# Performance work log

Hardware: AMD Instinct MI355X
Metric: run time of the kernel (lower is better)

Reference implementation:

```python
import jax, jax.numpy as jnp
import numpy as np
from jax import lax

# Conv3d(in_dim, in_dim, kernel=(1,3,3), padding=(0,1,1)) == per-time-slice 3x3 conv mixing channels

def _conv3d(x, w, b):
    # x: [B, C, T, W, H], w: [O, I, 1, 3, 3], b: [O]
    y = lax.conv_general_dilated(
        x, w,
        window_strides=(1, 1, 1),
        padding=[(0, 0), (1, 1), (1, 1)],
        dimension_numbers=("NCDHW", "OIDHW", "NCDHW"),
    )
    return y + b[None, :, None, None, None]


def setup_inputs() -> dict:
    key = jax.random.key(0)
    ks = jax.random.split(key, 8)
    B, C, T, W, H = 8, 64, 16, 64, 64
    fan = C * 1 * 3 * 3
    bound = 1.0 / np.sqrt(fan)  # torch Conv3d default init range
    x = jax.random.normal(ks[0], (B, C, T, W, H), dtype=jnp.float32)
    wq = jax.random.uniform(ks[1], (C, C, 1, 3, 3), jnp.float32, -bound, bound)
    wk = jax.random.uniform(ks[2], (C, C, 1, 3, 3), jnp.float32, -bound, bound)
    wv = jax.random.uniform(ks[3], (C, C, 1, 3, 3), jnp.float32, -bound, bound)
    bq = jax.random.uniform(ks[4], (C,), jnp.float32, -bound, bound)
    bk = jax.random.uniform(ks[5], (C,), jnp.float32, -bound, bound)
    bv = jax.random.uniform(ks[6], (C,), jnp.float32, -bound, bound)
    # torch init is gamma=0 (identity output); use nonzero so reference exercises the full path
    gamma = jax.random.normal(ks[7], (1,), dtype=jnp.float32) * 0.1
    return {"x": x, "wq": wq, "wk": wk, "wv": wv,
            "bq": bq, "bk": bk, "bv": bv, "gamma": gamma}


def reference(x, wq, wk, wv, bq, bk, bv, gamma):
    B, C, T, W, H = x.shape
    WH = W * H
    q = _conv3d(x, wq, bq).reshape(B, C, T, WH)
    k = _conv3d(x, wk, bk).reshape(B, C, T, WH)
    v = _conv3d(x, wv, bv).reshape(B, C, T, WH)
    # Original: (q[...,:,None] @ k[...,None,:]) @ v[...,:,None]  -> rank-1 energy, no softmax.
    # Exact reassociation: out_i = q_i * sum_j(k_j * v_j), avoiding the [WH, WH] matrix.
    s = jnp.sum(k * v, axis=-1, keepdims=True)  # [B, C, T, 1]
    out = (q * s).reshape(B, C, T, W, H)
    return gamma[0] * out + x
```

## Files before the change

### kernel.cpp

```cpp
#include <hip/hip_runtime.h>
#include <hip/hip_bf16.h>
#include <stdint.h>

typedef __attribute__((ext_vector_type(8))) short bf16x8;
typedef __attribute__((ext_vector_type(4))) float f32x4v;
typedef __attribute__((ext_vector_type(16))) float f32x16;

#define CH_STRIDE 65536

__device__ __forceinline__ uint16_t f2bf(float f) {
  uint32_t u = __builtin_bit_cast(uint32_t, f);
  u = (u + 0x7FFFu + ((u >> 16) & 1u)) >> 16;
  return (uint16_t)u;
}
__device__ __forceinline__ float bf2f(uint32_t b) {
  return __builtin_bit_cast(float, b << 16);
}
__device__ __forceinline__ uint16_t cvt_bf(float f) {
  return __builtin_bit_cast(uint16_t, __float2bfloat16(f));
}

#define MFMA32(a, b, c) __builtin_amdgcn_mfma_f32_32x32x16_bf16(a, b, c, 0, 0, 0)
#define WAIT0 asm volatile("s_waitcnt vmcnt(0) lgkmcnt(0)" ::: "memory")
#define BAR __builtin_amdgcn_s_barrier()
#define SCHED0 __builtin_amdgcn_sched_barrier(0)

#define LDSX6  (6 * 8 * 66 * 16)
#define LDSX10 (10 * 8 * 66 * 16)

__device__ __forceinline__ void gld16(const void* g, void* l) {
  __builtin_amdgcn_global_load_lds(
      (const __attribute__((address_space(1))) uint32_t*)g,
      (__attribute__((address_space(3))) uint32_t*)l, 16, 0, 0);
}

__device__ __forceinline__ bf16x8 ldx(const uint8_t* ldsx, int row, int oct, int ci) {
  return *(const bf16x8*)(ldsx + (uint32_t)((row * 8 + oct) * 66 + ci) * 16u);
}
__device__ __forceinline__ bf16x8 ldw_kv(const uint8_t* ldsw, int oct, int rowloc) {
  return *(const bf16x8*)(ldsw + (uint32_t)(oct * 128 + rowloc) * 16u);
}
__device__ __forceinline__ bf16x8 ldw_q(const uint8_t* ldsw, int oct, int row) {
  return *(const bf16x8*)(ldsw + (uint32_t)(oct * 64 + row) * 16u);
}

__device__ __forceinline__ void stage_unit(uint8_t* ldsx, const float* xs, int w0, int u) {
  int row = u >> 7, oct = (u >> 4) & 7, g = u & 15;
  int w = w0 - 1 + row;
  uint32_t base = (uint32_t)((row * 8 + oct) * 66 + 4 * g + 1) * 16u;
  if ((unsigned)w < 64u) {
    const float* p = xs + (size_t)(oct * 8) * CH_STRIDE + w * 64 + 4 * g;
    f32x4v v[8];
    #pragma unroll
    for (int j = 0; j < 8; ++j) v[j] = *(const f32x4v*)(p + (size_t)j * CH_STRIDE);
    #pragma unroll
    for (int c = 0; c < 4; ++c) {
      bf16x8 frag;
      #pragma unroll
      for (int q = 0; q < 4; ++q) {
        frag[2 * q]     = (short)cvt_bf(v[2 * q][c]);
        frag[2 * q + 1] = (short)cvt_bf(v[2 * q + 1][c]);
      }
      *(bf16x8*)(ldsx + base + (uint32_t)c * 16u) = frag;
    }
  } else {
    bf16x8 z = {};
    #pragma unroll
    for (int c = 0; c < 4; ++c) *(bf16x8*)(ldsx + base + (uint32_t)c * 16u) = z;
  }
}
__device__ __forceinline__ void stage_halo(uint8_t* ldsx, int tid, int nrow) {
  if (tid < nrow * 16) {
    int row = tid >> 4, rem = tid & 15;
    int oct = rem >> 1, side = rem & 1;
    bf16x8 z = {};
    *(bf16x8*)(ldsx + (uint32_t)((row * 8 + oct) * 66 + side * 65) * 16u) = z;
  }
}

__global__ void prep_weights(const float* __restrict__ wq, const float* __restrict__ wk,
                             const float* __restrict__ wv, uint16_t* __restrict__ wout) {
  int i = blockIdx.x * 256 + threadIdx.x;
  if (i >= 110592) return;
  if (i < 36864) {
    int tap = i >> 12, oct = (i >> 9) & 7, row = (i >> 3) & 63, j = i & 7;
    wout[i] = f2bf(wq[(row * 64 + oct * 8 + j) * 9 + tap]);
  } else {
    int m = i - 36864;
    int tap = m >> 13, oct = (m >> 10) & 7, rl = (m >> 3) & 127, j = m & 7;
    const float* src = (rl < 64) ? wk : wv;
    wout[i] = f2bf(src[((rl & 63) * 64 + oct * 8 + j) * 9 + tap]);
  }
}

__global__ __launch_bounds__(512, 2) void kv_s_kernel(
    const float* __restrict__ x, const uint16_t* __restrict__ wkv,
    const float* __restrict__ bk, const float* __restrict__ bv,
    float* __restrict__ s_out) {
  extern __shared__ uint8_t lds[];
  uint8_t* ldsx = lds;
  uint8_t* ldswA = lds + LDSX10;
  uint8_t* ldswB = lds + LDSX10 + 16384;
  const int tid = threadIdx.x;
  const int l = tid & 63;
  const int ng = tid >> 6;
  int bid = (int)(blockIdx.x & 7) * 128 + (int)(blockIdx.x >> 3);
  const int rg = bid & 7, slice = bid >> 3;
  const int b = slice >> 4, t = slice & 15;
  const int w0 = rg * 8;
  const float* xs = x + ((size_t)b * 1024 + t) * 4096;
  const int lm = l & 31, lh = l >> 5;

  gld16(wkv + (size_t)tid * 8, ldswA + (uint32_t)tid * 16u);
  gld16(wkv + (size_t)(tid + 512) * 8, ldswA + (uint32_t)(tid + 512) * 16u);
  stage_halo(ldsx, tid, 10);
  #pragma unroll
  for (int k = 0; k < 3; ++k) {
    int u = tid + k * 512;
    if (u < 1280) stage_unit(ldsx, xs, w0, u);
  }
  SCHED0; WAIT0; BAR; SCHED0;

  f32x16 accK[2][2], accV[2][2];
  #pragma unroll
  for (int mt = 0; mt < 2; ++mt)
    #pragma unroll
    for (int nt = 0; nt < 2; ++nt)
      #pragma unroll
      for (int q = 0; q < 16; ++q) { accK[mt][nt][q] = 0.f; accV[mt][nt][q] = 0.f; }

  #pragma unroll
  for (int tap = 0; tap < 9; ++tap) {
    const int dy = tap / 3, dx = tap % 3;
    const uint8_t* bufc = (tap & 1) ? ldswB : ldswA;
    uint8_t* bufn = (tap & 1) ? ldswA : ldswB;
    if (tap < 8) {
      gld16(wkv + ((size_t)(tap + 1) * 1024 + tid) * 8, bufn + (uint32_t)tid * 16u);
      gld16(wkv + ((size_t)(tap + 1) * 1024 + tid + 512) * 8,
            bufn + (uint32_t)(tid + 512) * 16u);
    }
    __builtin_amdgcn_s_setprio(1);
    #pragma unroll
    for (int s = 0; s < 4; ++s) {
      int oct = s * 2 + lh;
      bf16x8 aK0 = ldw_kv(bufc, oct, lm);
      bf16x8 aK1 = ldw_kv(bufc, oct, 32 + lm);
      bf16x8 aV0 = ldw_kv(bufc, oct, 64 + lm);
      bf16x8 aV1 = ldw_kv(bufc, oct, 96 + lm);
      bf16x8 b0  = ldx(ldsx, ng + dy, oct, lm + dx);
      bf16x8 b1  = ldx(ldsx, ng + dy, oct, 32 + lm + dx);
      accK[0][0] = MFMA32(aK0, b0, accK[0][0]);
      accK[0][1] = MFMA32(aK0, b1, accK[0][1]);
      accK[1][0] = MFMA32(aK1, b0, accK[1][0]);
      accK[1][1] = MFMA32(aK1, b1, accK[1][1]);
      accV[0][0] = MFMA32(aV0, b0, accV[0][0]);
      accV[0][1] = MFMA32(aV0, b1, accV[0][1]);
      accV[1][0] = MFMA32(aV1, b0, accV[1][0]);
      accV[1][1] = MFMA32(aV1, b1, accV[1][1]);
    }
    __builtin_amdgcn_s_setprio(0);
    SCHED0; WAIT0; BAR; SCHED0;
  }

  __syncthreads();
  float* red = (float*)lds;
  #pragma unroll
  for (int q = 0; q < 16; ++q) {
    int cl = (q & 3) + 8 * (q >> 2) + 4 * lh;
    #pragma unroll
    for (int mt = 0; mt < 2; ++mt) {
      int c = mt * 32 + cl;
      float bkc = bk[c], bvc = bv[c];
      float p = (accK[mt][0][q] + bkc) * (accV[mt][0][q] + bvc)
              + (accK[mt][1][q] + bkc) * (accV[mt][1][q] + bvc);
      red[c * 261 + ng * 32 + lm] = p;
    }
  }
  __syncthreads();
  if (tid < 64) {
    const float* rp = red + tid * 261;
    f32x4v a4 = {0.f, 0.f, 0.f, 0.f};
    #pragma unroll
    for (int j = 0; j < 64; ++j) a4 += *(const f32x4v*)(rp + j * 4);
    atomicAdd(s_out + (b * 16 + t) * 64 + tid, a4[0] + a4[1] + a4[2] + a4[3]);
  }
}

__global__ __launch_bounds__(256, 2) void q_out_kernel(
    const float* __restrict__ x, const uint16_t* __restrict__ wq,
    const float* __restrict__ bq, const float* __restrict__ s_in,
    const float* __restrict__ gamma, float* __restrict__ out) {
  extern __shared__ uint8_t lds[];
  uint8_t* ldsx = lds;
  uint8_t* ldswA = lds + LDSX6;
  uint8_t* ldswB = lds + LDSX6 + 8192;
  const int tid = threadIdx.x;
  const int l = tid & 63, ng = tid >> 6;
  int bid = (int)(blockIdx.x & 7) * 256 + (int)(blockIdx.x >> 3);
  const int rg = bid & 15, slice = bid >> 4;
  const int b = slice >> 4, t = slice & 15;
  const int w0 = rg * 4;
  const float* xs = x + ((size_t)b * 1024 + t) * 4096;
  const int lm = l & 31, lh = l >> 5;

  #pragma unroll
  for (int k = 0; k < 2; ++k)
    gld16(wq + (size_t)(tid + k * 256) * 8, ldswA + (uint32_t)(tid + k * 256) * 16u);
  stage_halo(ldsx, tid, 6);
  #pragma unroll
  for (int k = 0; k < 3; ++k) stage_unit(ldsx, xs, w0, tid + k * 256);
  SCHED0; WAIT0; BAR; SCHED0;

  f32x16 acc[2][2];
  #pragma unroll
  for (int mt = 0; mt < 2; ++mt)
    #pragma unroll
    for (int nt = 0; nt < 2; ++nt)
      #pragma unroll
      for (int q = 0; q < 16; ++q) acc[mt][nt][q] = 0.f;

  #pragma unroll
  for (int tap = 0; tap < 9; ++tap) {
    const int dy = tap / 3, dx = tap % 3;
    const uint8_t* bufc = (tap & 1) ? ldswB : ldswA;
    uint8_t* bufn = (tap & 1) ? ldswA : ldswB;
    if (tap < 8) {
      #pragma unroll
      for (int k = 0; k < 2; ++k)
        gld16(wq + ((size_t)(tap + 1) * 512 + tid + k * 256) * 8,
              bufn + (uint32_t)(tid + k * 256) * 16u);
    }
    __builtin_amdgcn_s_setprio(1);
    #pragma unroll
    for (int s = 0; s < 4; ++s) {
      int oct = s * 2 + lh;
      bf16x8 a0 = ldw_q(bufc, oct, lm);
      bf16x8 a1 = ldw_q(bufc, oct, 32 + lm);
      bf16x8 b0 = ldx(ldsx, ng + dy, oct, lm + dx);
      bf16x8 b1 = ldx(ldsx, ng + dy, oct, 32 + lm + dx);
      acc[0][0] = MFMA32(a0, b0, acc[0][0]);
      acc[0][1] = MFMA32(a0, b1, acc[0][1]);
      acc[1][0] = MFMA32(a1, b0, acc[1][0]);
      acc[1][1] = MFMA32(a1, b1, acc[1][1]);
    }
    __builtin_amdgcn_s_setprio(0);
    SCHED0; WAIT0; BAR; SCHED0;
  }

  float g = gamma[0];
  const float* sb = s_in + (b * 16 + t) * 64;
  int w = w0 + ng;
  #pragma unroll
  for (int mt = 0; mt < 2; ++mt) {
    #pragma unroll
    for (int q = 0; q < 16; ++q) {
      int cl = (q & 3) + 8 * (q >> 2) + 4 * lh;
      int c  = mt * 32 + cl;
      float qb = bq[c], sc = sb[c];
      #pragma unroll
      for (int nt = 0; nt < 2; ++nt) {
        int h = nt * 32 + lm;
        uint32_t xb = (uint32_t)(((ng + 1) * 8 + (c >> 3)) * 66 + (h + 1)) * 16u
                    + (uint32_t)(c & 7) * 2u;
        float xv = bf2f(*(const uint16_t*)(ldsx + xb));
        size_t idx = ((size_t)(b * 64 + c) * 16 + t) * 4096 + (size_t)w * 64 + h;
        out[idx] = g * (acc[mt][nt][q] + qb) * sc + xv;
      }
    }
  }
}

extern "C" void kernel_launch(void* const* d_in, const int* in_sizes, int n_in,
                              void* d_out, int out_size, void* d_ws, size_t ws_size,
                              hipStream_t stream) {
  const float* x   = (const float*)d_in[0];
  const float* wq  = (const float*)d_in[1];
  const float* wk  = (const float*)d_in[2];
  const float* wv  = (const float*)d_in[3];
  const float* bq  = (const float*)d_in[4];
  const float* bk  = (const float*)d_in[5];
  const float* bv  = (const float*)d_in[6];
  const float* gam = (const float*)d_in[7];

  uint16_t* wbf = (uint16_t*)d_ws;
  float* sbuf   = (float*)((uint8_t*)d_ws + 221184);

  hipMemsetAsync(sbuf, 0, 8 * 16 * 64 * sizeof(float), stream);
  prep_weights<<<(110592 + 255) / 256, 256, 0, stream>>>(wq, wk, wv, wbf);
  kv_s_kernel<<<1024, 512, LDSX10 + 32768, stream>>>(x, wbf + 36864, bk, bv, sbuf);
  q_out_kernel<<<2048, 256, LDSX6 + 16384, stream>>>(x, wbf, bq, sbuf, gam, (float*)d_out);
}
```

Measured before the change: 153.2 us.

## Shrink kv conv tile to 4 rows and replace LDS halo with wraparound masking

The K/V conv kernel now processes 4 output rows per block with 256 threads instead of 8 rows with 512 threads, which doubles the grid to 2048 blocks. The x tile in LDS drops its 66-column halo padding for a 64-column layout. Edge columns are handled by wrapping the column index and zeroing the wrapped fragment with a per-lane bitmask. This cuts LDS per block and may raise occupancy. In exchange, each block re-stages more halo rows relative to useful rows, reloads the full K/V weight set per block, and issues twice as many atomics.

```diff
diff --git a/kernel.cpp b/kernel.cpp
--- a/kernel.cpp
+++ b/kernel.cpp
@@ -5,6 +5,7 @@
 typedef __attribute__((ext_vector_type(8))) short bf16x8;
 typedef __attribute__((ext_vector_type(4))) float f32x4v;
 typedef __attribute__((ext_vector_type(16))) float f32x16;
+typedef __attribute__((ext_vector_type(4))) unsigned int u32x4;
 
 #define CH_STRIDE 65536
 
@@ -19,6 +20,11 @@
 __device__ __forceinline__ uint16_t cvt_bf(float f) {
   return __builtin_bit_cast(uint16_t, __float2bfloat16(f));
 }
+__device__ __forceinline__ bf16x8 andm(bf16x8 v, uint32_t m) {
+  u32x4 u = __builtin_bit_cast(u32x4, v);
+  u[0] &= m; u[1] &= m; u[2] &= m; u[3] &= m;
+  return __builtin_bit_cast(bf16x8, u);
+}
 
 #define MFMA32(a, b, c) __builtin_amdgcn_mfma_f32_32x32x16_bf16(a, b, c, 0, 0, 0)
 #define WAIT0 asm volatile("s_waitcnt vmcnt(0) lgkmcnt(0)" ::: "memory")
@@ -26,7 +32,7 @@
 #define SCHED0 __builtin_amdgcn_sched_barrier(0)
 
 #define LDSX6  (6 * 8 * 66 * 16)
-#define LDSX10 (10 * 8 * 66 * 16)
+#define LDSK   (6 * 8 * 64 * 16)
 
 __device__ __forceinline__ void gld16(const void* g, void* l) {
   __builtin_amdgcn_global_load_lds(
@@ -37,6 +43,9 @@
 __device__ __forceinline__ bf16x8 ldx(const uint8_t* ldsx, int row, int oct, int ci) {
   return *(const bf16x8*)(ldsx + (uint32_t)((row * 8 + oct) * 66 + ci) * 16u);
 }
+__device__ __forceinline__ bf16x8 ldx64(const uint8_t* ldsx, int row, int oct, int ci) {
+  return *(const bf16x8*)(ldsx + (uint32_t)((row * 8 + oct) * 64 + ci) * 16u);
+}
 __device__ __forceinline__ bf16x8 ldw_kv(const uint8_t* ldsw, int oct, int rowloc) {
   return *(const bf16x8*)(ldsw + (uint32_t)(oct * 128 + rowloc) * 16u);
 }
@@ -44,7 +53,7 @@
   return *(const bf16x8*)(ldsw + (uint32_t)(oct * 64 + row) * 16u);
 }
 
-__device__ __forceinline__ void stage_unit(uint8_t* ldsx, const float* xs, int w0, int u) {
+__device__ __forceinline__ void stage_unit66(uint8_t* ldsx, const float* xs, int w0, int u) {
   int row = u >> 7, oct = (u >> 4) & 7, g = u & 15;
   int w = w0 - 1 + row;
   uint32_t base = (uint32_t)((row * 8 + oct) * 66 + 4 * g + 1) * 16u;
@@ -69,7 +78,32 @@
     for (int c = 0; c < 4; ++c) *(bf16x8*)(ldsx + base + (uint32_t)c * 16u) = z;
   }
 }
-__device__ __forceinline__ void stage_halo(uint8_t* ldsx, int tid, int nrow) {
+__device__ __forceinline__ void stage_unit64(uint8_t* ldsx, const float* xs, int w0, int u) {
+  int row = u >> 7, oct = (u >> 4) & 7, g = u & 15;
+  int w = w0 - 1 + row;
+  uint32_t base = (uint32_t)((row * 8 + oct) * 64 + 4 * g) * 16u;
+  if ((unsigned)w < 64u) {
+    const float* p = xs + (size_t)(oct * 8) * CH_STRIDE + w * 64 + 4 * g;
+    f32x4v v[8];
+    #pragma unroll
+    for (int j = 0; j < 8; ++j) v[j] = *(const f32x4v*)(p + (size_t)j * CH_STRIDE);
+    #pragma unroll
+    for (int c = 0; c < 4; ++c) {
+      bf16x8 frag;
+      #pragma unroll
+      for (int q = 0; q < 4; ++q) {
+        frag[2 * q]     = (short)cvt_bf(v[2 * q][c]);
+        frag[2 * q + 1] = (short)cvt_bf(v[2 * q + 1][c]);
+      }
+      *(bf16x8*)(ldsx + base + (uint32_t)c * 16u) = frag;
+    }
+  } else {
+    bf16x8 z = {};
+    #pragma unroll
+    for (int c = 0; c < 4; ++c) *(bf16x8*)(ldsx + base + (uint32_t)c * 16u) = z;
+  }
+}
+__device__ __forceinline__ void stage_halo66(uint8_t* ldsx, int tid, int nrow) {
   if (tid < nrow * 16) {
     int row = tid >> 4, rem = tid & 15;
     int oct = rem >> 1, side = rem & 1;
@@ -93,32 +127,31 @@
   }
 }
 
-__global__ __launch_bounds__(512, 2) void kv_s_kernel(
+__global__ __launch_bounds__(256, 2) void kv_s_kernel(
     const float* __restrict__ x, const uint16_t* __restrict__ wkv,
     const float* __restrict__ bk, const float* __restrict__ bv,
     float* __restrict__ s_out) {
   extern __shared__ uint8_t lds[];
   uint8_t* ldsx = lds;
-  uint8_t* ldswA = lds + LDSX10;
-  uint8_t* ldswB = lds + LDSX10 + 16384;
+  uint8_t* ldswA = lds + LDSK;
+  uint8_t* ldswB = lds + LDSK + 16384;
   const int tid = threadIdx.x;
   const int l = tid & 63;
   const int ng = tid >> 6;
-  int bid = (int)(blockIdx.x & 7) * 128 + (int)(blockIdx.x >> 3);
-  const int rg = bid & 7, slice = bid >> 3;
+  int bid = (int)(blockIdx.x & 7) * 256 + (int)(blockIdx.x >> 3);
+  const int rg = bid & 15, slice = bid >> 4;
   const int b = slice >> 4, t = slice & 15;
-  const int w0 = rg * 8;
+  const int w0 = rg * 4;
   const float* xs = x + ((size_t)b * 1024 + t) * 4096;
   const int lm = l & 31, lh = l >> 5;
-
-  gld16(wkv + (size_t)tid * 8, ldswA + (uint32_t)tid * 16u);
-  gld16(wkv + (size_t)(tid + 512) * 8, ldswA + (uint32_t)(tid + 512) * 16u);
-  stage_halo(ldsx, tid, 10);
-  #pragma unroll
-  for (int k = 0; k < 3; ++k) {
-    int u = tid + k * 512;
-    if (u < 1280) stage_unit(ldsx, xs, w0, u);
-  }
+  const uint32_t mz0 = (lm == 0) ? 0u : ~0u;
+  const uint32_t mz1 = (lm == 31) ? 0u : ~0u;
+
+  #pragma unroll
+  for (int k = 0; k < 4; ++k)
+    gld16(wkv + (size_t)(tid + k * 256) * 8, ldswA + (uint32_t)(tid + k * 256) * 16u);
+  #pragma unroll
+  for (int k = 0; k < 3; ++k) stage_unit64(ldsx, xs, w0, tid + k * 256);
   SCHED0; WAIT0; BAR; SCHED0;
 
   f32x16 accK[2][2], accV[2][2];
@@ -135,9 +168,10 @@
     const uint8_t* bufc = (tap & 1) ? ldswB : ldswA;
     uint8_t* bufn = (tap & 1) ? ldswA : ldswB;
     if (tap < 8) {
-      gld16(wkv + ((size_t)(tap + 1) * 1024 + tid) * 8, bufn + (uint32_t)tid * 16u);
-      gld16(wkv + ((size_t)(tap + 1) * 1024 + tid + 512) * 8,
-            bufn + (uint32_t)(tid + 512) * 16u);
+      #pragma unroll
+      for (int k = 0; k < 4; ++k)
+        gld16(wkv + ((size_t)(tap + 1) * 1024 + tid + k * 256) * 8,
+              bufn + (uint32_t)(tid + k * 256) * 16u);
     }
     __builtin_amdgcn_s_setprio(1);
     #pragma unroll
@@ -147,8 +181,10 @@
       bf16x8 aK1 = ldw_kv(bufc, oct, 32 + lm);
       bf16x8 aV0 = ldw_kv(bufc, oct, 64 + lm);
       bf16x8 aV1 = ldw_kv(bufc, oct, 96 + lm);
-      bf16x8 b0  = ldx(ldsx, ng + dy, oct, lm + dx);
-      bf16x8 b1  = ldx(ldsx, ng + dy, oct, 32 + lm + dx);
+      bf16x8 b0  = ldx64(ldsx, ng + dy, oct, (lm + dx - 1) & 63);
+      bf16x8 b1  = ldx64(ldsx, ng + dy, oct, (32 + lm + dx - 1) & 63);
+      if (dx == 0) b0 = andm(b0, mz0);
+      if (dx == 2) b1 = andm(b1, mz1);
       accK[0][0] = MFMA32(aK0, b0, accK[0][0]);
       accK[0][1] = MFMA32(aK0, b1, accK[0][1]);
       accK[1][0] = MFMA32(aK1, b0, accK[1][0]);
@@ -173,15 +209,15 @@
       float bkc = bk[c], bvc = bv[c];
       float p = (accK[mt][0][q] + bkc) * (accV[mt][0][q] + bvc)
               + (accK[mt][1][q] + bkc) * (accV[mt][1][q] + bvc);
-      red[c * 261 + ng * 32 + lm] = p;
+      red[c * 133 + ng * 32 + lm] = p;
     }
   }
   __syncthreads();
   if (tid < 64) {
-    const float* rp = red + tid * 261;
+    const float* rp = red + tid * 133;
     f32x4v a4 = {0.f, 0.f, 0.f, 0.f};
     #pragma unroll
-    for (int j = 0; j < 64; ++j) a4 += *(const f32x4v*)(rp + j * 4);
+    for (int j = 0; j < 32; ++j) a4 += *(const f32x4v*)(rp + j * 4);
     atomicAdd(s_out + (b * 16 + t) * 64 + tid, a4[0] + a4[1] + a4[2] + a4[3]);
   }
 }
@@ -206,9 +242,9 @@
   #pragma unroll
   for (int k = 0; k < 2; ++k)
     gld16(wq + (size_t)(tid + k * 256) * 8, ldswA + (uint32_t)(tid + k * 256) * 16u);
-  stage_halo(ldsx, tid, 6);
-  #pragma unroll
-  for (int k = 0; k < 3; ++k) stage_unit(ldsx, xs, w0, tid + k * 256);
+  stage_halo66(ldsx, tid, 6);
+  #pragma unroll
+  for (int k = 0; k < 3; ++k) stage_unit66(ldsx, xs, w0, tid + k * 256);
   SCHED0; WAIT0; BAR; SCHED0;
 
   f32x16 acc[2][2];
@@ -287,6 +323,6 @@
 
   hipMemsetAsync(sbuf, 0, 8 * 16 * 64 * sizeof(float), stream);
   prep_weights<<<(110592 + 255) / 256, 256, 0, stream>>>(wq, wk, wv, wbf);
-  kv_s_kernel<<<1024, 512, LDSX10 + 32768, stream>>>(x, wbf + 36864, bk, bv, sbuf);
+  kv_s_kernel<<<2048, 256, LDSK + 32768, stream>>>(x, wbf + 36864, bk, bv, sbuf);
   q_out_kernel<<<2048, 256, LDSX6 + 16384, stream>>>(x, wbf, bq, sbuf, gam, (float*)d_out);
 }
```

New measurement: 149.8 us, median of 2. 2.2% less time.
